# Kernel tuning notes

Measured on AMD Instinct MI355X. Metric: run time of the kernel, lower is better.

The kernel has to match this reference:

```python
import jax, jax.numpy as jnp
import numpy as np

B, N, C, H, P = 8, 4096, 256, 4, 64  # batch, tokens, hidden, heads, proj_size


def setup_inputs() -> dict:
    key = jax.random.key(0)
    ks = jax.random.split(key, 6)
    sc = 0.02
    x = jax.random.normal(ks[0], (B, N, C), jnp.float32)
    bank = jax.random.normal(ks[1], (B, N, C), jnp.float32)  # unused by forward, kept for fidelity
    W_qkvv = jax.random.normal(ks[2], (4 * C, C), jnp.float32) * sc  # Linear(C, 4C), no bias
    W_E = jax.random.normal(ks[3], (P, N), jnp.float32) * sc          # E = F shared Linear(N, P)
    b_E = jnp.zeros((P,), jnp.float32)
    temperature = jnp.ones((H, 1, 1), jnp.float32)
    temperature2 = jnp.ones((H, 1, 1), jnp.float32)
    W_out1 = jax.random.normal(ks[4], (C // 2, C), jnp.float32) * sc  # out_proj (spatial branch)
    b_out1 = jnp.zeros((C // 2,), jnp.float32)
    W_out2 = jax.random.normal(ks[5], (C // 2, C), jnp.float32) * sc  # out_proj2 (channel branch)
    b_out2 = jnp.zeros((C // 2,), jnp.float32)
    prelu_a = jnp.array(0.25, jnp.float32)  # nn.PReLU() default: single shared slope
    return {"x": x, "bank": bank, "W_qkvv": W_qkvv, "W_E": W_E, "b_E": b_E,
            "temperature": temperature, "temperature2": temperature2,
            "W_out1": W_out1, "b_out1": b_out1, "W_out2": W_out2, "b_out2": b_out2,
            "prelu_a": prelu_a}


def _l2norm(t):
    # torch F.normalize(dim=-1): x / max(||x||_2, eps)
    return t / jnp.maximum(jnp.linalg.norm(t, axis=-1, keepdims=True), 1e-12)


def reference(x, bank, W_qkvv, W_E, b_E, temperature, temperature2,
              W_out1, b_out1, W_out2, b_out2, prelu_a):
    Bb, Nn, Cc = x.shape
    Hh = temperature.shape[0]
    d = Cc // Hh
    # qkvv projection -> [4, B, H, N, d], then transpose token/feature axes -> [B, H, d, N]
    qkvv = (x @ W_qkvv.T).reshape(Bb, Nn, 4, Hh, d).transpose(2, 0, 3, 1, 4)
    q, k, v_ca, v_sa = (qkvv[0].transpose(0, 1, 3, 2), qkvv[1].transpose(0, 1, 3, 2),
                        qkvv[2].transpose(0, 1, 3, 2), qkvv[3].transpose(0, 1, 3, 2))
    # shared linear E=F projects the token axis N -> P (applied to UNnormalized k, v_sa)
    k_proj = jnp.einsum('bhdn,pn->bhdp', k, W_E) + b_E      # [B,H,d,P]
    v_sa_proj = jnp.einsum('bhdn,pn->bhdp', v_sa, W_E) + b_E  # [B,H,d,P]
    qn = _l2norm(q)
    kn = _l2norm(k)
    # channel attention: [B,H,d,d]
    attn_ca = jax.nn.softmax(jnp.einsum('bhdn,bhen->bhde', qn, kn) * temperature, axis=-1)
    x_ca = jnp.einsum('bhde,bhen->bhdn', attn_ca, v_ca).transpose(0, 3, 1, 2).reshape(Bb, Nn, Cc)
    # spatial attention (projected): [B,H,N,P]
    attn_sa = jax.nn.softmax(jnp.einsum('bhdn,bhdp->bhnp', qn, k_proj) * temperature2, axis=-1)
    x_sa = jnp.einsum('bhnp,bhdp->bhnd', attn_sa, v_sa_proj).transpose(0, 2, 1, 3).reshape(Bb, Nn, Cc)
    x_sa = x_sa @ W_out1.T + b_out1
    x_ca = x_ca @ W_out2.T + b_out2
    out = jnp.concatenate([x_sa, x_ca], axis=-1)
    return jnp.where(out >= 0, out, prelu_a * out)  # PReLU
```

## Files before the change

### kernel.cpp

```cpp
#include <hip/hip_runtime.h>
#include <cstdint>
#include <cstddef>

constexpr int B_ = 8, N_ = 4096, C_ = 256, H_ = 4, D_ = 64, P_ = 64;
constexpr int OC_ = 4 * C_;
constexpr int M_  = B_ * N_;
constexpr int GX_ROWS = 320;
constexpr int KS_G = 8;
constexpr int XT_TILES = M_ / 64;

#define DEV_INLINE __device__ __forceinline__

typedef unsigned short ushort_t;
typedef __attribute__((ext_vector_type(8))) short short8;
typedef __attribute__((ext_vector_type(4))) short short4v;
typedef __attribute__((ext_vector_type(4))) float floatx4;

DEV_INLINE short f2bf(float f) {
  unsigned int u = __builtin_bit_cast(unsigned int, f);
  u += 0x7FFFu + ((u >> 16) & 1u);
  return (short)(u >> 16);
}
DEV_INLINE float bf2f(ushort_t u) {
  return __builtin_bit_cast(float, (unsigned int)u << 16);
}
DEV_INLINE short4v cvt4(float4 v) {
  short4v s = {f2bf(v.x), f2bf(v.y), f2bf(v.z), f2bf(v.w)};
  return s;
}

__global__ __launch_bounds__(256) void k_cast(const float* __restrict__ x,
                                              const float* __restrict__ Wq,
                                              const float* __restrict__ WE,
                                              const float* __restrict__ W1,
                                              const float* __restrict__ W2,
                                              ushort_t* __restrict__ xt,
                                              ushort_t* __restrict__ wqb,
                                              ushort_t* __restrict__ web,
                                              ushort_t* __restrict__ w1b,
                                              ushort_t* __restrict__ w2b) {
  const int t = threadIdx.x;
  if (blockIdx.x >= XT_TILES) {
    constexpr size_t WQ4 = (size_t)OC_ * C_ / 4;
    constexpr size_t WE4 = (size_t)P_ * N_ / 4;
    constexpr size_t W14 = (size_t)128 * C_ / 4;
    constexpr size_t TOTW4 = WQ4 + WE4 + 2 * W14;
    const size_t stride = (size_t)128 * 256;
    for (size_t i = (size_t)(blockIdx.x - XT_TILES) * 256 + t; i < TOTW4; i += stride) {
      const float* src; ushort_t* dst; size_t o;
      if (i < WQ4) { src = Wq; dst = wqb; o = i; }
      else if (i < WQ4 + WE4) { src = WE; dst = web; o = i - WQ4; }
      else if (i < WQ4 + WE4 + W14) { src = W1; dst = w1b; o = i - WQ4 - WE4; }
      else { src = W2; dst = w2b; o = i - WQ4 - WE4 - W14; }
      float4 v = ((const float4*)src)[o];
      *(short4v*)&dst[o * 4] = cvt4(v);
    }
    return;
  }
  __shared__ __align__(16) short Xs[64 * 264];
  const int n0 = blockIdx.x * 64;
  const int b = n0 >> 12, nl = n0 & 4095;
#pragma unroll
  for (int rep = 0; rep < 16; ++rep) {
    const int f4 = rep * 256 + t;
    const int row = f4 >> 6, c4 = f4 & 63;
    float4 v = *(const float4*)&x[(size_t)(n0 + row) * 256 + c4 * 4];
    *(short4v*)&Xs[row * 264 + c4 * 4] = cvt4(v);
  }
  __syncthreads();
  const int ch = t;
  ushort_t* dst = &xt[((size_t)b * 256 + ch) * 4096 + nl];
#pragma unroll
  for (int g = 0; g < 8; ++g) {
    short8 o;
#pragma unroll
    for (int i = 0; i < 8; ++i) o[i] = Xs[(g * 8 + i) * 264 + ch];
    *(short8*)&dst[g * 8] = o;
  }
}

__global__ __launch_bounds__(512) void k_gram(const ushort_t* __restrict__ xt,
                                              const ushort_t* __restrict__ web,
                                              float* __restrict__ Gxp) {
  __shared__ __align__(16) short As[128 * 72];
  __shared__ __align__(16) short Bs[256 * 72];
  const int job = blockIdx.x;
  const int y = blockIdx.y;
  const int b = y >> 3, ksp = y & 7;
  const int t = threadIdx.x;
  const int oc = t & 7, rr = t >> 3;
  const int lane = t & 63, wave = t >> 6;
  const int m16 = lane & 15, quad = lane >> 4;
  const int wm = (wave >> 2) << 6, wn = (wave & 3) << 6;
  const ushort_t* Asrc = (job < 2)
      ? xt + (size_t)(b * 256 + job * 128) * 4096 : web;
  const ushort_t* Bsrc = xt + (size_t)b * 256 * 4096;
  floatx4 acc[4][4];
#pragma unroll
  for (int i = 0; i < 4; ++i)
#pragma unroll
    for (int j = 0; j < 4; ++j) acc[i][j] = (floatx4)(0.f);
#pragma unroll 1
  for (int it = 0; it < 8; ++it) {
    const int n0 = ksp * 512 + it * 64;
    short8 a8[2], b8[4];
#pragma unroll
    for (int rp = 0; rp < 2; ++rp) {
      int ar = rr + 64 * rp;
      if (job == 2) ar &= 63;
      a8[rp] = *(const short8*)&Asrc[(size_t)ar * 4096 + n0 + 8 * oc];
    }
#pragma unroll
    for (int rp = 0; rp < 4; ++rp)
      b8[rp] = *(const short8*)&Bsrc[(size_t)(rr + 64 * rp) * 4096 + n0 + 8 * oc];
    __syncthreads();
#pragma unroll
    for (int rp = 0; rp < 2; ++rp)
      *(short8*)&As[(rr + 64 * rp) * 72 + 8 * oc] = a8[rp];
#pragma unroll
    for (int rp = 0; rp < 4; ++rp)
      *(short8*)&Bs[(rr + 64 * rp) * 72 + 8 * oc] = b8[rp];
    __syncthreads();
#pragma unroll
    for (int ks = 0; ks < 2; ++ks) {
      if (job < 2) {
        short8 af[4], bf[4];
#pragma unroll
        for (int i = 0; i < 4; ++i)
          af[i] = *(const short8*)&As[(wm + i * 16 + m16) * 72 + ks * 32 + quad * 8];
#pragma unroll
        for (int j = 0; j < 4; ++j)
          bf[j] = *(const short8*)&Bs[(wn + j * 16 + m16) * 72 + ks * 32 + quad * 8];
#pragma unroll
        for (int i = 0; i < 4; ++i)
#pragma unroll
          for (int j = 0; j < 4; ++j)
            acc[i][j] = __builtin_amdgcn_mfma_f32_16x16x32_bf16(af[i], bf[j], acc[i][j], 0, 0, 0);
      } else {
        short8 af[4], bf[2];
#pragma unroll
        for (int i = 0; i < 4; ++i)
          af[i] = *(const short8*)&As[(i * 16 + m16) * 72 + ks * 32 + quad * 8];
#pragma unroll
        for (int j = 0; j < 2; ++j)
          bf[j] = *(const short8*)&Bs[(wave * 32 + j * 16 + m16) * 72 + ks * 32 + quad * 8];
#pragma unroll
        for (int i = 0; i < 4; ++i)
#pragma unroll
          for (int j = 0; j < 2; ++j)
            acc[i][j] = __builtin_amdgcn_mfma_f32_16x16x32_bf16(af[i], bf[j], acc[i][j], 0, 0, 0);
      }
    }
  }
  float* pb = Gxp + (size_t)y * (GX_ROWS * 256);
  if (job < 2) {
#pragma unroll
    for (int i = 0; i < 4; ++i)
#pragma unroll
      for (int r = 0; r < 4; ++r) {
        const int grow = job * 128 + wm + i * 16 + quad * 4 + r;
#pragma unroll
        for (int j = 0; j < 4; ++j)
          pb[(size_t)grow * 256 + wn + j * 16 + m16] = acc[i][j][r];
      }
  } else {
#pragma unroll
    for (int i = 0; i < 4; ++i)
#pragma unroll
      for (int r = 0; r < 4; ++r) {
        const int grow = 256 + i * 16 + quad * 4 + r;
#pragma unroll
        for (int j = 0; j < 2; ++j)
          pb[(size_t)grow * 256 + wave * 32 + j * 16 + m16] = acc[i][j][r];
      }
  }
}

__global__ __launch_bounds__(256) void k_gred(const float* __restrict__ Gxp,
                                              float* __restrict__ Gx) {
  const int i = blockIdx.x * 256 + threadIdx.x;
  constexpr int PB4 = GX_ROWS * 256 / 4;
  const int fb = i / PB4, rem = i - fb * PB4;
  const float4* p = (const float4*)Gxp;
  float4 s = p[(size_t)fb * KS_G * PB4 + rem];
#pragma unroll
  for (int k = 1; k < KS_G; ++k) {
    float4 v = p[((size_t)fb * KS_G + k) * PB4 + rem];
    s.x += v.x; s.y += v.y; s.z += v.z; s.w += v.w;
  }
  ((float4*)Gx)[i] = s;
}

__global__ __launch_bounds__(256) void k_mid1(const ushort_t* __restrict__ wqb,
                                              const float* __restrict__ Gx,
                                              ushort_t* __restrict__ T2b,
                                              float* __restrict__ ssq) {
  __shared__ __align__(16) short As[128 * 72];
  __shared__ __align__(16) short Bs[128 * 72];
  const int bm = blockIdx.x * 128;
  const int b  = blockIdx.y >> 1;
  const int jb = blockIdx.y & 1;
  const int t = threadIdx.x;
  const int oc = t & 7;
  const int rr = t >> 3;
  const int lane = t & 63, wave = t >> 6;
  const int m16 = lane & 15, quad = lane >> 4;
  const int wm = (wave >> 1) << 6, wn = (wave & 1) << 6;
  const float* Bsrc = Gx + ((size_t)b * GX_ROWS + jb * 128) * 256;
  floatx4 acc[4][4];
#pragma unroll
  for (int i = 0; i < 4; ++i)
#pragma unroll
    for (int j = 0; j < 4; ++j) acc[i][j] = (floatx4)(0.f);
#pragma unroll 1
  for (int k0 = 0; k0 < 256; k0 += 64) {
    short8 a8[4], b8[4];
#pragma unroll
    for (int j = 0; j < 4; ++j) {
      const int r = rr + 32 * j;
      a8[j] = *(const short8*)&wqb[(size_t)(bm + r) * 256 + k0 + 8 * oc];
      float4 g0 = *(const float4*)&Bsrc[(size_t)r * 256 + k0 + 8 * oc];
      float4 g1 = *(const float4*)&Bsrc[(size_t)r * 256 + k0 + 8 * oc + 4];
      short8 bb;
      bb[0] = f2bf(g0.x); bb[1] = f2bf(g0.y); bb[2] = f2bf(g0.z); bb[3] = f2bf(g0.w);
      bb[4] = f2bf(g1.x); bb[5] = f2bf(g1.y); bb[6] = f2bf(g1.z); bb[7] = f2bf(g1.w);
      b8[j] = bb;
    }
    __syncthreads();
#pragma unroll
    for (int j = 0; j < 4; ++j) {
      const int r = rr + 32 * j;
      *(short8*)&As[r * 72 + 8 * oc] = a8[j];
      *(short8*)&Bs[r * 72 + 8 * oc] = b8[j];
    }
    __syncthreads();
#pragma unroll
    for (int ks = 0; ks < 2; ++ks) {
      short8 af[4], bf[4];
#pragma unroll
      for (int i = 0; i < 4; ++i)
        af[i] = *(const short8*)&As[(wm + i * 16 + m16) * 72 + ks * 32 + quad * 8];
#pragma unroll
      for (int j = 0; j < 4; ++j)
        bf[j] = *(const short8*)&Bs[(wn + j * 16 + m16) * 72 + ks * 32 + quad * 8];
#pragma unroll
      for (int i = 0; i < 4; ++i)
#pragma unroll
        for (int j = 0; j < 4; ++j)
          acc[i][j] = __builtin_amdgcn_mfma_f32_16x16x32_bf16(af[i], bf[j], acc[i][j], 0, 0, 0);
    }
  }
#pragma unroll
  for (int i = 0; i < 4; ++i)
#pragma unroll
    for (int r = 0; r < 4; ++r) {
      const int gr = bm + wm + i * 16 + quad * 4 + r;
      float s = 0.f;
#pragma unroll
      for (int j = 0; j < 4; ++j) {
        const int col = jb * 128 + wn + j * 16 + m16;
        T2b[((size_t)b * 512 + gr) * 256 + col] = (ushort_t)f2bf(acc[i][j][r]);
        s += bf2f(wqb[(size_t)gr * 256 + col]) * acc[i][j][r];
      }
      s += __shfl_xor(s, 1);
      s += __shfl_xor(s, 2);
      s += __shfl_xor(s, 4);
      s += __shfl_xor(s, 8);
      if (m16 == 0) atomicAdd(&ssq[b * 512 + gr], s);
    }
}

__global__ __launch_bounds__(256) void k_mid2(const ushort_t* __restrict__ wqb,
                                              const ushort_t* __restrict__ T2b,
                                              const float* __restrict__ Gx,
                                              const float* __restrict__ ssq,
                                              const float* __restrict__ bE,
                                              const float* __restrict__ t1,
                                              const float* __restrict__ t2,
                                              ushort_t* __restrict__ ab,
                                              ushort_t* __restrict__ ksb,
                                              ushort_t* __restrict__ vsb) {
  const int bh = blockIdx.x;
  const int job = blockIdx.y;
  const int b = bh >> 2, h = bh & 3;
  const int wave = threadIdx.x >> 6;
  const int lane = threadIdx.x & 63;
  const int m16 = lane & 15, quad = lane >> 4;
  const int Abase = (job == 0 ? 0 : (job == 1 ? 256 : 768)) + h * 64;
  const int arow = Abase + 16 * wave + m16;
  floatx4 acc[4];
#pragma unroll
  for (int j = 0; j < 4; ++j) acc[j] = (floatx4)(0.f);
#pragma unroll
  for (int ks = 0; ks < 8; ++ks) {
    const int boct = ks * 32 + quad * 8;
    short8 af = *(const short8*)&wqb[(size_t)arow * 256 + boct];
    short8 bf[4];
    if (job == 0) {
#pragma unroll
      for (int j = 0; j < 4; ++j)
        bf[j] = *(const short8*)&T2b[((size_t)b * 512 + 256 + h * 64 + 16 * j + m16) * 256 + boct];
    } else {
#pragma unroll
      for (int j = 0; j < 4; ++j) {
        const float* gp = Gx + ((size_t)b * GX_ROWS + 256 + 16 * j + m16) * 256 + boct;
        float4 g0 = *(const float4*)gp;
        float4 g1 = *(const float4*)(gp + 4);
        short8 bb;
        bb[0] = f2bf(g0.x); bb[1] = f2bf(g0.y); bb[2] = f2bf(g0.z); bb[3] = f2bf(g0.w);
        bb[4] = f2bf(g1.x); bb[5] = f2bf(g1.y); bb[6] = f2bf(g1.z); bb[7] = f2bf(g1.w);
        bf[j] = bb;
      }
    }
#pragma unroll
    for (int j = 0; j < 4; ++j)
      acc[j] = __builtin_amdgcn_mfma_f32_16x16x32_bf16(af, bf[j], acc[j], 0, 0, 0);
  }
  if (job == 0) {
    const float t1h = t1[h];
    float rnk[4];
#pragma unroll
    for (int j = 0; j < 4; ++j)
      rnk[j] = 1.f / fmaxf(sqrtf(ssq[b * 512 + 256 + h * 64 + 16 * j + m16]), 1e-12f);
#pragma unroll
    for (int r = 0; r < 4; ++r) {
      const int d = 16 * wave + quad * 4 + r;
      const float rq = 1.f / fmaxf(sqrtf(ssq[b * 512 + h * 64 + d]), 1e-12f);
      float l[4];
      float m = -1e30f;
#pragma unroll
      for (int j = 0; j < 4; ++j) {
        l[j] = acc[j][r] * rq * rnk[j] * t1h;
        m = fmaxf(m, l[j]);
      }
      m = fmaxf(m, __shfl_xor(m, 1));
      m = fmaxf(m, __shfl_xor(m, 2));
      m = fmaxf(m, __shfl_xor(m, 4));
      m = fmaxf(m, __shfl_xor(m, 8));
      float s = 0.f;
#pragma unroll
      for (int j = 0; j < 4; ++j) {
        l[j] = __expf(l[j] - m);
        s += l[j];
      }
      s += __shfl_xor(s, 1);
      s += __shfl_xor(s, 2);
      s += __shfl_xor(s, 4);
      s += __shfl_xor(s, 8);
      const float inv = 1.f / s;
#pragma unroll
      for (int j = 0; j < 4; ++j)
        ab[(size_t)bh * 4096 + d * 64 + 16 * j + m16] = (ushort_t)f2bf(l[j] * inv);
    }
  } else if (job == 1) {
    const float tt = t2[h];
#pragma unroll
    for (int r = 0; r < 4; ++r) {
      const int d = 16 * wave + quad * 4 + r;
      const float rq = 1.f / fmaxf(sqrtf(ssq[b * 512 + h * 64 + d]), 1e-12f);
#pragma unroll
      for (int j = 0; j < 4; ++j) {
        const int p = 16 * j + m16;
        ksb[(size_t)bh * 4096 + p * 64 + d] =
            (ushort_t)f2bf((acc[j][r] + bE[p]) * rq * tt);
      }
    }
  } else {
#pragma unroll
    for (int r = 0; r < 4; ++r) {
      const int d = 16 * wave + quad * 4 + r;
#pragma unroll
      for (int j = 0; j < 4; ++j) {
        const int p = 16 * j + m16;
        vsb[(size_t)bh * 4096 + d * 64 + p] = (ushort_t)f2bf(acc[j][r] + bE[p]);
      }
    }
  }
}

__global__ __launch_bounds__(256) void k_tok(const float* __restrict__ x,
                                             const ushort_t* __restrict__ wqb,
                                             const ushort_t* __restrict__ ab,
                                             const ushort_t* __restrict__ ksb,
                                             const ushort_t* __restrict__ vsb,
                                             const ushort_t* __restrict__ w1b,
                                             const float* __restrict__ b1,
                                             const ushort_t* __restrict__ w2b,
                                             const float* __restrict__ b2,
                                             const float* __restrict__ pa,
                                             float* __restrict__ out) {
  __shared__ __align__(16) short Xs[64 * 264];
  __shared__ __align__(16) short Qs[64 * 264];
  __shared__ __align__(16) short Vs[64 * 264];
  const int n0 = blockIdx.x * 64;
  const int b = n0 >> 12;
  const int t = threadIdx.x;
  const int lane = t & 63, wave = t >> 6;
  const int m16 = lane & 15, quad = lane >> 4;
  const int cw = wave * 64;
#pragma unroll
  for (int rep = 0; rep < 16; ++rep) {
    const int f4 = rep * 256 + t;
    const int row = f4 >> 6, c4 = f4 & 63;
    float4 v = *(const float4*)&x[(size_t)(n0 + row) * 256 + c4 * 4];
    *(short4v*)&Xs[row * 264 + c4 * 4] = cvt4(v);
  }
  __syncthreads();
#pragma unroll 1
  for (int pass = 0; pass < 2; ++pass) {
    const int wrow = (pass ? 512 : 0) + cw;
    short* dst = pass ? Vs : Qs;
    floatx4 acc[4][4];
#pragma unroll
    for (int i = 0; i < 4; ++i)
#pragma unroll
      for (int j = 0; j < 4; ++j) acc[i][j] = (floatx4)(0.f);
#pragma unroll
    for (int ks = 0; ks < 8; ++ks) {
      const int boct = ks * 32 + quad * 8;
      short8 af[4], bf[4];
#pragma unroll
      for (int i = 0; i < 4; ++i)
        af[i] = *(const short8*)&Xs[(16 * i + m16) * 264 + boct];
#pragma unroll
      for (int j = 0; j < 4; ++j)
        bf[j] = *(const short8*)&wqb[(size_t)(wrow + 16 * j + m16) * 256 + boct];
#pragma unroll
      for (int i = 0; i < 4; ++i)
#pragma unroll
        for (int j = 0; j < 4; ++j)
          acc[i][j] = __builtin_amdgcn_mfma_f32_16x16x32_bf16(af[i], bf[j], acc[i][j], 0, 0, 0);
    }
#pragma unroll
    for (int i = 0; i < 4; ++i)
#pragma unroll
      for (int r = 0; r < 4; ++r)
#pragma unroll
        for (int j = 0; j < 4; ++j)
          dst[(16 * i + quad * 4 + r) * 264 + cw + 16 * j + m16] =
              (short)f2bf(acc[i][j][r]);
  }
  __syncthreads();
  const int bh = b * 4 + wave;
  {
    floatx4 s[4][4];
#pragma unroll
    for (int i = 0; i < 4; ++i)
#pragma unroll
      for (int j = 0; j < 4; ++j) s[i][j] = (floatx4)(0.f);
#pragma unroll
    for (int ks = 0; ks < 2; ++ks) {
      const int boct = ks * 32 + quad * 8;
      short8 af[4], bf[4];
#pragma unroll
      for (int i = 0; i < 4; ++i)
        af[i] = *(const short8*)&Qs[(16 * i + m16) * 264 + cw + boct];
#pragma unroll
      for (int j = 0; j < 4; ++j)
        bf[j] = *(const short8*)&ksb[(size_t)bh * 4096 + (16 * j + m16) * 64 + boct];
#pragma unroll
      for (int i = 0; i < 4; ++i)
#pragma unroll
        for (int j = 0; j < 4; ++j)
          s[i][j] = __builtin_amdgcn_mfma_f32_16x16x32_bf16(af[i], bf[j], s[i][j], 0, 0, 0);
    }
#pragma unroll
    for (int i = 0; i < 4; ++i)
#pragma unroll
      for (int r = 0; r < 4; ++r) {
        float mr = fmaxf(fmaxf(s[i][0][r], s[i][1][r]), fmaxf(s[i][2][r], s[i][3][r]));
        mr = fmaxf(mr, __shfl_xor(mr, 1));
        mr = fmaxf(mr, __shfl_xor(mr, 2));
        mr = fmaxf(mr, __shfl_xor(mr, 4));
        mr = fmaxf(mr, __shfl_xor(mr, 8));
        float sr = 0.f;
#pragma unroll
        for (int j = 0; j < 4; ++j) {
          const float e = __expf(s[i][j][r] - mr);
          s[i][j][r] = e;
          sr += e;
        }
        sr += __shfl_xor(sr, 1);
        sr += __shfl_xor(sr, 2);
        sr += __shfl_xor(sr, 4);
        sr += __shfl_xor(sr, 8);
        const float inv = 1.f / sr;
#pragma unroll
        for (int j = 0; j < 4; ++j) s[i][j][r] *= inv;
      }
#pragma unroll
    for (int i = 0; i < 4; ++i)
#pragma unroll
      for (int r = 0; r < 4; ++r)
#pragma unroll
        for (int j = 0; j < 4; ++j)
          Qs[(16 * i + quad * 4 + r) * 264 + cw + 16 * j + m16] =
              (short)f2bf(s[i][j][r]);
    floatx4 o[4][4];
#pragma unroll
    for (int i = 0; i < 4; ++i)
#pragma unroll
      for (int j = 0; j < 4; ++j) o[i][j] = (floatx4)(0.f);
#pragma unroll
    for (int ks = 0; ks < 2; ++ks) {
      const int boct = ks * 32 + quad * 8;
      short8 af[4], bf[4];
#pragma unroll
      for (int i = 0; i < 4; ++i)
        af[i] = *(const short8*)&Qs[(16 * i + m16) * 264 + cw + boct];
#pragma unroll
      for (int j = 0; j < 4; ++j)
        bf[j] = *(const short8*)&vsb[(size_t)bh * 4096 + (16 * j + m16) * 64 + boct];
#pragma unroll
      for (int i = 0; i < 4; ++i)
#pragma unroll
        for (int j = 0; j < 4; ++j)
          o[i][j] = __builtin_amdgcn_mfma_f32_16x16x32_bf16(af[i], bf[j], o[i][j], 0, 0, 0);
    }
#pragma unroll
    for (int i = 0; i < 4; ++i)
#pragma unroll
      for (int r = 0; r < 4; ++r)
#pragma unroll
        for (int j = 0; j < 4; ++j)
          Xs[(16 * i + quad * 4 + r) * 264 + cw + 16 * j + m16] =
              (short)f2bf(o[i][j][r]);
  }
  {
    floatx4 o[4][4];
#pragma unroll
    for (int i = 0; i < 4; ++i)
#pragma unroll
      for (int j = 0; j < 4; ++j) o[i][j] = (floatx4)(0.f);
#pragma unroll
    for (int ks = 0; ks < 2; ++ks) {
      const int boct = ks * 32 + quad * 8;
      short8 af[4], bf[4];
#pragma unroll
      for (int i = 0; i < 4; ++i)
        af[i] = *(const short8*)&Vs[(16 * i + m16) * 264 + cw + boct];
#pragma unroll
      for (int j = 0; j < 4; ++j)
        bf[j] = *(const short8*)&ab[(size_t)bh * 4096 + (16 * j + m16) * 64 + boct];
#pragma unroll
      for (int i = 0; i < 4; ++i)
#pragma unroll
        for (int j = 0; j < 4; ++j)
          o[i][j] = __builtin_amdgcn_mfma_f32_16x16x32_bf16(af[i], bf[j], o[i][j], 0, 0, 0);
    }
#pragma unroll
    for (int i = 0; i < 4; ++i)
#pragma unroll
      for (int r = 0; r < 4; ++r)
#pragma unroll
        for (int j = 0; j < 4; ++j)
          Vs[(16 * i + quad * 4 + r) * 264 + cw + 16 * j + m16] =
              (short)f2bf(o[i][j][r]);
  }
  __syncthreads();
  {
    const short* Asrc = (wave < 2) ? Xs : Vs;
    const ushort_t* Wsrc = (wave < 2) ? w1b : w2b;
    const float* bias = (wave < 2) ? b1 : b2;
    const int wrow = (wave & 1) * 64;
    const int colbase = (wave < 2 ? 0 : 128) + wrow;
    floatx4 acc[4][4];
#pragma unroll
    for (int i = 0; i < 4; ++i)
#pragma unroll
      for (int j = 0; j < 4; ++j) acc[i][j] = (floatx4)(0.f);
#pragma unroll
    for (int ks = 0; ks < 8; ++ks) {
      const int boct = ks * 32 + quad * 8;
      short8 af[4], bf[4];
#pragma unroll
      for (int i = 0; i < 4; ++i)
        af[i] = *(const short8*)&Asrc[(16 * i + m16) * 264 + boct];
#pragma unroll
      for (int j = 0; j < 4; ++j)
        bf[j] = *(const short8*)&Wsrc[(size_t)(wrow + 16 * j + m16) * 256 + boct];
#pragma unroll
      for (int i = 0; i < 4; ++i)
#pragma unroll
        for (int j = 0; j < 4; ++j)
          acc[i][j] = __builtin_amdgcn_mfma_f32_16x16x32_bf16(af[i], bf[j], acc[i][j], 0, 0, 0);
    }
    const float slope = pa[0];
    float bj[4];
#pragma unroll
    for (int j = 0; j < 4; ++j) bj[j] = bias[wrow + 16 * j + m16];
#pragma unroll
    for (int i = 0; i < 4; ++i)
#pragma unroll
      for (int r = 0; r < 4; ++r) {
        const int gr = n0 + 16 * i + quad * 4 + r;
#pragma unroll
        for (int j = 0; j < 4; ++j) {
          float v = acc[i][j][r] + bj[j];
          v = v >= 0.f ? v : slope * v;
          out[(size_t)gr * C_ + colbase + 16 * j + m16] = v;
        }
      }
  }
}

extern "C" void kernel_launch(void* const* d_in, const int* in_sizes, int n_in,
                              void* d_out, int out_size, void* d_ws, size_t ws_size,
                              hipStream_t stream) {
  (void)in_sizes; (void)n_in; (void)out_size; (void)ws_size;
  const float* x  = (const float*)d_in[0];
  const float* Wq = (const float*)d_in[2];
  const float* WE = (const float*)d_in[3];
  const float* bE = (const float*)d_in[4];
  const float* t1 = (const float*)d_in[5];
  const float* t2 = (const float*)d_in[6];
  const float* W1 = (const float*)d_in[7];
  const float* b1 = (const float*)d_in[8];
  const float* W2 = (const float*)d_in[9];
  const float* b2 = (const float*)d_in[10];
  const float* pa = (const float*)d_in[11];
  float* out = (float*)d_out;

  float* ws = (float*)d_ws;
  size_t off = 0;
  float* Gx  = ws + off; off += (size_t)B_ * GX_ROWS * 256;
  float* ssq = ws + off; off += (size_t)B_ * 512;
  float* Gxp = ws + off; off += (size_t)KS_G * B_ * GX_ROWS * 256;
  ushort_t* ksb = (ushort_t*)(ws + off); off += 32 * 4096 / 2;
  ushort_t* vsb = (ushort_t*)(ws + off); off += 32 * 4096 / 2;
  ushort_t* ab  = (ushort_t*)(ws + off); off += 32 * 4096 / 2;
  ushort_t* xt  = (ushort_t*)(ws + off); off += (size_t)M_ * C_ / 2;
  ushort_t* wqb = (ushort_t*)(ws + off); off += (size_t)OC_ * C_ / 2;
  ushort_t* w1b = (ushort_t*)(ws + off); off += (size_t)128 * C_ / 2;
  ushort_t* w2b = (ushort_t*)(ws + off); off += (size_t)128 * C_ / 2;
  ushort_t* web = (ushort_t*)(ws + off); off += (size_t)P_ * N_ / 2;
  ushort_t* T2b = (ushort_t*)(ws + off); off += (size_t)B_ * 512 * C_ / 2;

  hipMemsetAsync(ssq, 0, (size_t)B_ * 512 * sizeof(float), stream);

  k_cast<<<XT_TILES + 128, 256, 0, stream>>>(x, Wq, WE, W1, W2,
                                             xt, wqb, web, w1b, w2b);
  k_gram<<<dim3(3, B_ * KS_G), 512, 0, stream>>>(xt, web, Gxp);
  k_gred<<<GX_ROWS * 256 * B_ / 4 / 256, 256, 0, stream>>>(Gxp, Gx);
  k_mid1<<<dim3(4, B_ * 2), 256, 0, stream>>>(wqb, Gx, T2b, ssq);
  k_mid2<<<dim3(32, 3), 256, 0, stream>>>(wqb, T2b, Gx, ssq, bE, t1, t2, ab, ksb, vsb);
  k_tok<<<M_ / 64, 256, 0, stream>>>(x, wqb, ab, ksb, vsb, w1b, b1, w2b, b2, pa, out);
}
```

Measured before the change: 227.5 us.

## Cut k_tok shared memory to two buffers and request two blocks per CU

Shared memory in the token kernel drops from three 64x264 bf16 buffers to two. The Q projection and spatial attention now run first, writing into Ys. The V_ca projection is then computed from Xs and overwrites Xs after a barrier. This lowers LDS per block and adds a launch-bounds minimum of two blocks, aiming for higher occupancy, but it reorders the stages and forces the compiler to fit registers under the tighter bound, which could cause spills.

```diff
diff --git a/kernel.cpp b/kernel.cpp
--- a/kernel.cpp
+++ b/kernel.cpp
@@ -378,26 +378,26 @@
   }
 }
 
-__global__ __launch_bounds__(256) void k_tok(const float* __restrict__ x,
-                                             const ushort_t* __restrict__ wqb,
-                                             const ushort_t* __restrict__ ab,
-                                             const ushort_t* __restrict__ ksb,
-                                             const ushort_t* __restrict__ vsb,
-                                             const ushort_t* __restrict__ w1b,
-                                             const float* __restrict__ b1,
-                                             const ushort_t* __restrict__ w2b,
-                                             const float* __restrict__ b2,
-                                             const float* __restrict__ pa,
-                                             float* __restrict__ out) {
+__global__ __launch_bounds__(256, 2) void k_tok(const float* __restrict__ x,
+                                                const ushort_t* __restrict__ wqb,
+                                                const ushort_t* __restrict__ ab,
+                                                const ushort_t* __restrict__ ksb,
+                                                const ushort_t* __restrict__ vsb,
+                                                const ushort_t* __restrict__ w1b,
+                                                const float* __restrict__ b1,
+                                                const ushort_t* __restrict__ w2b,
+                                                const float* __restrict__ b2,
+                                                const float* __restrict__ pa,
+                                                float* __restrict__ out) {
   __shared__ __align__(16) short Xs[64 * 264];
-  __shared__ __align__(16) short Qs[64 * 264];
-  __shared__ __align__(16) short Vs[64 * 264];
+  __shared__ __align__(16) short Ys[64 * 264];
   const int n0 = blockIdx.x * 64;
   const int b = n0 >> 12;
   const int t = threadIdx.x;
   const int lane = t & 63, wave = t >> 6;
   const int m16 = lane & 15, quad = lane >> 4;
   const int cw = wave * 64;
+  const int bh = b * 4 + wave;
 #pragma unroll
   for (int rep = 0; rep < 16; ++rep) {
     const int f4 = rep * 256 + t;
@@ -406,10 +406,7 @@
     *(short4v*)&Xs[row * 264 + c4 * 4] = cvt4(v);
   }
   __syncthreads();
-#pragma unroll 1
-  for (int pass = 0; pass < 2; ++pass) {
-    const int wrow = (pass ? 512 : 0) + cw;
-    short* dst = pass ? Vs : Qs;
+  {
     floatx4 acc[4][4];
 #pragma unroll
     for (int i = 0; i < 4; ++i)
@@ -424,7 +421,7 @@
         af[i] = *(const short8*)&Xs[(16 * i + m16) * 264 + boct];
 #pragma unroll
       for (int j = 0; j < 4; ++j)
-        bf[j] = *(const short8*)&wqb[(size_t)(wrow + 16 * j + m16) * 256 + boct];
+        bf[j] = *(const short8*)&wqb[(size_t)(cw + 16 * j + m16) * 256 + boct];
 #pragma unroll
       for (int i = 0; i < 4; ++i)
 #pragma unroll
@@ -437,11 +434,9 @@
       for (int r = 0; r < 4; ++r)
 #pragma unroll
         for (int j = 0; j < 4; ++j)
-          dst[(16 * i + quad * 4 + r) * 264 + cw + 16 * j + m16] =
+          Ys[(16 * i + quad * 4 + r) * 264 + cw + 16 * j + m16] =
               (short)f2bf(acc[i][j][r]);
   }
-  __syncthreads();
-  const int bh = b * 4 + wave;
   {
     floatx4 s[4][4];
 #pragma unroll
@@ -454,7 +449,7 @@
       short8 af[4], bf[4];
 #pragma unroll
       for (int i = 0; i < 4; ++i)
-        af[i] = *(const short8*)&Qs[(16 * i + m16) * 264 + cw + boct];
+        af[i] = *(const short8*)&Ys[(16 * i + m16) * 264 + cw + boct];
 #pragma unroll
       for (int j = 0; j < 4; ++j)
         bf[j] = *(const short8*)&ksb[(size_t)bh * 4096 + (16 * j + m16) * 64 + boct];
@@ -494,7 +489,7 @@
       for (int r = 0; r < 4; ++r)
 #pragma unroll
         for (int j = 0; j < 4; ++j)
-          Qs[(16 * i + quad * 4 + r) * 264 + cw + 16 * j + m16] =
+          Ys[(16 * i + quad * 4 + r) * 264 + cw + 16 * j + m16] =
               (short)f2bf(s[i][j][r]);
     floatx4 o[4][4];
 #pragma unroll
@@ -507,7 +502,7 @@
       short8 af[4], bf[4];
 #pragma unroll
       for (int i = 0; i < 4; ++i)
-        af[i] = *(const short8*)&Qs[(16 * i + m16) * 264 + cw + boct];
+        af[i] = *(const short8*)&Ys[(16 * i + m16) * 264 + cw + boct];
 #pragma unroll
       for (int j = 0; j < 4; ++j)
         bf[j] = *(const short8*)&vsb[(size_t)bh * 4096 + (16 * j + m16) * 64 + boct];
@@ -523,9 +518,39 @@
       for (int r = 0; r < 4; ++r)
 #pragma unroll
         for (int j = 0; j < 4; ++j)
-          Xs[(16 * i + quad * 4 + r) * 264 + cw + 16 * j + m16] =
+          Ys[(16 * i + quad * 4 + r) * 264 + cw + 16 * j + m16] =
               (short)f2bf(o[i][j][r]);
   }
+  floatx4 accv[4][4];
+#pragma unroll
+  for (int i = 0; i < 4; ++i)
+#pragma unroll
+    for (int j = 0; j < 4; ++j) accv[i][j] = (floatx4)(0.f);
+#pragma unroll
+  for (int ks = 0; ks < 8; ++ks) {
+    const int boct = ks * 32 + quad * 8;
+    short8 af[4], bf[4];
+#pragma unroll
+    for (int i = 0; i < 4; ++i)
+      af[i] = *(const short8*)&Xs[(16 * i + m16) * 264 + boct];
+#pragma unroll
+    for (int j = 0; j < 4; ++j)
+      bf[j] = *(const short8*)&wqb[(size_t)(512 + cw + 16 * j + m16) * 256 + boct];
+#pragma unroll
+    for (int i = 0; i < 4; ++i)
+#pragma unroll
+      for (int j = 0; j < 4; ++j)
+        accv[i][j] = __builtin_amdgcn_mfma_f32_16x16x32_bf16(af[i], bf[j], accv[i][j], 0, 0, 0);
+  }
+  __syncthreads();
+#pragma unroll
+  for (int i = 0; i < 4; ++i)
+#pragma unroll
+    for (int r = 0; r < 4; ++r)
+#pragma unroll
+      for (int j = 0; j < 4; ++j)
+        Xs[(16 * i + quad * 4 + r) * 264 + cw + 16 * j + m16] =
+            (short)f2bf(accv[i][j][r]);
   {
     floatx4 o[4][4];
 #pragma unroll
@@ -538,7 +563,7 @@
       short8 af[4], bf[4];
 #pragma unroll
       for (int i = 0; i < 4; ++i)
-        af[i] = *(const short8*)&Vs[(16 * i + m16) * 264 + cw + boct];
+        af[i] = *(const short8*)&Xs[(16 * i + m16) * 264 + cw + boct];
 #pragma unroll
       for (int j = 0; j < 4; ++j)
         bf[j] = *(const short8*)&ab[(size_t)bh * 4096 + (16 * j + m16) * 64 + boct];
@@ -554,12 +579,12 @@
       for (int r = 0; r < 4; ++r)
 #pragma unroll
         for (int j = 0; j < 4; ++j)
-          Vs[(16 * i + quad * 4 + r) * 264 + cw + 16 * j + m16] =
+          Xs[(16 * i + quad * 4 + r) * 264 + cw + 16 * j + m16] =
               (short)f2bf(o[i][j][r]);
   }
   __syncthreads();
   {
-    const short* Asrc = (wave < 2) ? Xs : Vs;
+    const short* Asrc = (wave < 2) ? Ys : Xs;
     const ushort_t* Wsrc = (wave < 2) ? w1b : w2b;
     const float* bias = (wave < 2) ? b1 : b2;
     const int wrow = (wave & 1) * 64;
```

Result: faster. 214.5 us (-5.7%).

## Fold Q and V_ca projections into per-batch weights, removing token-level qkvv GEMM

Applied to the files above, without the earlier changes.

Precomputes per-(batch,head) combined matrices: the scaled K projection is multiplied by W_q (Kc), and the channel-attention matrix by W_v and then by W_out2 (M2). The token kernel can then compute spatial scores directly from X and the channel branch directly from X with M2, skipping the 64x512x256 qkvv GEMM per tile. It also drops one LDS buffer and sets launch_bounds occupancy to 2. The cost is two small extra kernels, a larger K dimension in the score GEMM (256 instead of 64), and different bf16 rounding points.

```diff
diff --git a/kernel.cpp b/kernel.cpp
--- a/kernel.cpp
+++ b/kernel.cpp
@@ -38,8 +38,35 @@
                                               ushort_t* __restrict__ wqb,
                                               ushort_t* __restrict__ web,
                                               ushort_t* __restrict__ w1b,
-                                              ushort_t* __restrict__ w2b) {
+                                              ushort_t* __restrict__ w2b,
+                                              ushort_t* __restrict__ wqtq,
+                                              ushort_t* __restrict__ wv2t) {
+  __shared__ __align__(16) short Xs[64 * 264];
   const int t = threadIdx.x;
+  if (blockIdx.x >= XT_TILES + 128) {
+    const int tb = blockIdx.x - (XT_TILES + 128);
+    const int srcbase = (tb < 4 ? 0 : 512) + (tb & 3) * 64;
+    ushort_t* dstm = (tb < 4) ? wqtq : wv2t;
+    const int R = (tb & 3) * 64;
+#pragma unroll
+    for (int rep = 0; rep < 16; ++rep) {
+      const int f4 = rep * 256 + t;
+      const int row = f4 >> 6, c4 = f4 & 63;
+      float4 v = *(const float4*)&Wq[(size_t)(srcbase + row) * 256 + c4 * 4];
+      *(short4v*)&Xs[row * 264 + c4 * 4] = cvt4(v);
+    }
+    __syncthreads();
+    const int ch = t;
+    ushort_t* dst = &dstm[ch * 256 + R];
+#pragma unroll
+    for (int g = 0; g < 8; ++g) {
+      short8 o;
+#pragma unroll
+      for (int i = 0; i < 8; ++i) o[i] = Xs[(g * 8 + i) * 264 + ch];
+      *(short8*)&dst[g * 8] = o;
+    }
+    return;
+  }
   if (blockIdx.x >= XT_TILES) {
     constexpr size_t WQ4 = (size_t)OC_ * C_ / 4;
     constexpr size_t WE4 = (size_t)P_ * N_ / 4;
@@ -57,7 +84,6 @@
     }
     return;
   }
-  __shared__ __align__(16) short Xs[64 * 264];
   const int n0 = blockIdx.x * 64;
   const int b = n0 >> 12, nl = n0 & 4095;
 #pragma unroll
@@ -378,26 +404,118 @@
   }
 }
 
-__global__ __launch_bounds__(256) void k_tok(const float* __restrict__ x,
-                                             const ushort_t* __restrict__ wqb,
-                                             const ushort_t* __restrict__ ab,
-                                             const ushort_t* __restrict__ ksb,
-                                             const ushort_t* __restrict__ vsb,
-                                             const ushort_t* __restrict__ w1b,
-                                             const float* __restrict__ b1,
-                                             const ushort_t* __restrict__ w2b,
-                                             const float* __restrict__ b2,
-                                             const float* __restrict__ pa,
-                                             float* __restrict__ out) {
+__global__ __launch_bounds__(256) void k_mid3(const ushort_t* __restrict__ ksb,
+                                              const ushort_t* __restrict__ ab,
+                                              const ushort_t* __restrict__ wqtq,
+                                              const ushort_t* __restrict__ wv2t,
+                                              ushort_t* __restrict__ Kc,
+                                              ushort_t* __restrict__ AcT) {
+  const int bh = blockIdx.x;
+  const int job = blockIdx.y;
+  const int h = bh & 3;
+  const int wave = threadIdx.x >> 6;
+  const int lane = threadIdx.x & 63;
+  const int m16 = lane & 15, quad = lane >> 4;
+  const ushort_t* A = (job ? ab : ksb) + (size_t)bh * 4096;
+  const ushort_t* Bt = job ? wv2t : wqtq;
+  floatx4 acc[4][4];
+#pragma unroll
+  for (int i = 0; i < 4; ++i)
+#pragma unroll
+    for (int j = 0; j < 4; ++j) acc[i][j] = (floatx4)(0.f);
+#pragma unroll
+  for (int ks = 0; ks < 2; ++ks) {
+    const int boct = ks * 32 + quad * 8;
+    short8 af[4], bf[4];
+#pragma unroll
+    for (int i = 0; i < 4; ++i)
+      af[i] = *(const short8*)&A[(16 * i + m16) * 64 + boct];
+#pragma unroll
+    for (int j = 0; j < 4; ++j)
+      bf[j] = *(const short8*)&Bt[(size_t)(wave * 64 + 16 * j + m16) * 256 + h * 64 + boct];
+#pragma unroll
+    for (int i = 0; i < 4; ++i)
+#pragma unroll
+      for (int j = 0; j < 4; ++j)
+        acc[i][j] = __builtin_amdgcn_mfma_f32_16x16x32_bf16(af[i], bf[j], acc[i][j], 0, 0, 0);
+  }
+#pragma unroll
+  for (int i = 0; i < 4; ++i)
+#pragma unroll
+    for (int r = 0; r < 4; ++r) {
+      const int ar = 16 * i + quad * 4 + r;
+#pragma unroll
+      for (int j = 0; j < 4; ++j) {
+        const int cc = wave * 64 + 16 * j + m16;
+        if (job == 0)
+          Kc[(size_t)bh * 16384 + ar * 256 + cc] = (ushort_t)f2bf(acc[i][j][r]);
+        else
+          AcT[(size_t)bh * 16384 + cc * 64 + ar] = (ushort_t)f2bf(acc[i][j][r]);
+      }
+    }
+}
+
+__global__ __launch_bounds__(256) void k_mid4(const ushort_t* __restrict__ w2b,
+                                              const ushort_t* __restrict__ AcT,
+                                              ushort_t* __restrict__ M2) {
+  const int b = blockIdx.x;
+  const int ob = blockIdx.y * 64;
+  const int wave = threadIdx.x >> 6;
+  const int lane = threadIdx.x & 63;
+  const int m16 = lane & 15, quad = lane >> 4;
+  floatx4 acc[4][4];
+#pragma unroll
+  for (int i = 0; i < 4; ++i)
+#pragma unroll
+    for (int j = 0; j < 4; ++j) acc[i][j] = (floatx4)(0.f);
+#pragma unroll
+  for (int ks = 0; ks < 8; ++ks) {
+    const int boct = ks * 32 + quad * 8;
+    const int hsel = boct >> 6, de = boct & 63;
+    short8 af[4], bf[4];
+#pragma unroll
+    for (int i = 0; i < 4; ++i)
+      af[i] = *(const short8*)&w2b[(size_t)(ob + 16 * i + m16) * 256 + boct];
+#pragma unroll
+    for (int j = 0; j < 4; ++j)
+      bf[j] = *(const short8*)&AcT[((size_t)(b * 4 + hsel)) * 16384 +
+                                   (wave * 64 + 16 * j + m16) * 64 + de];
+#pragma unroll
+    for (int i = 0; i < 4; ++i)
+#pragma unroll
+      for (int j = 0; j < 4; ++j)
+        acc[i][j] = __builtin_amdgcn_mfma_f32_16x16x32_bf16(af[i], bf[j], acc[i][j], 0, 0, 0);
+  }
+#pragma unroll
+  for (int i = 0; i < 4; ++i)
+#pragma unroll
+    for (int r = 0; r < 4; ++r) {
+      const int oo = ob + 16 * i + quad * 4 + r;
+#pragma unroll
+      for (int j = 0; j < 4; ++j)
+        M2[(size_t)b * 32768 + oo * 256 + wave * 64 + 16 * j + m16] =
+            (ushort_t)f2bf(acc[i][j][r]);
+    }
+}
+
+__global__ __launch_bounds__(256, 2) void k_tok(const float* __restrict__ x,
+                                                const ushort_t* __restrict__ Kc,
+                                                const ushort_t* __restrict__ vsb,
+                                                const ushort_t* __restrict__ M2,
+                                                const ushort_t* __restrict__ w1b,
+                                                const float* __restrict__ b1,
+                                                const float* __restrict__ b2,
+                                                const float* __restrict__ pa,
+                                                float* __restrict__ out) {
   __shared__ __align__(16) short Xs[64 * 264];
-  __shared__ __align__(16) short Qs[64 * 264];
-  __shared__ __align__(16) short Vs[64 * 264];
+  __shared__ __align__(16) short Ys[64 * 264];
   const int n0 = blockIdx.x * 64;
   const int b = n0 >> 12;
   const int t = threadIdx.x;
   const int lane = t & 63, wave = t >> 6;
   const int m16 = lane & 15, quad = lane >> 4;
   const int cw = wave * 64;
+  const int bh = b * 4 + wave;
 #pragma unroll
   for (int rep = 0; rep < 16; ++rep) {
     const int f4 = rep * 256 + t;
@@ -406,15 +524,12 @@
     *(short4v*)&Xs[row * 264 + c4 * 4] = cvt4(v);
   }
   __syncthreads();
-#pragma unroll 1
-  for (int pass = 0; pass < 2; ++pass) {
-    const int wrow = (pass ? 512 : 0) + cw;
-    short* dst = pass ? Vs : Qs;
-    floatx4 acc[4][4];
-#pragma unroll
-    for (int i = 0; i < 4; ++i)
-#pragma unroll
-      for (int j = 0; j < 4; ++j) acc[i][j] = (floatx4)(0.f);
+  {
+    floatx4 s[4][4];
+#pragma unroll
+    for (int i = 0; i < 4; ++i)
+#pragma unroll
+      for (int j = 0; j < 4; ++j) s[i][j] = (floatx4)(0.f);
 #pragma unroll
     for (int ks = 0; ks < 8; ++ks) {
       const int boct = ks * 32 + quad * 8;
@@ -424,40 +539,7 @@
         af[i] = *(const short8*)&Xs[(16 * i + m16) * 264 + boct];
 #pragma unroll
       for (int j = 0; j < 4; ++j)
-        bf[j] = *(const short8*)&wqb[(size_t)(wrow + 16 * j + m16) * 256 + boct];
-#pragma unroll
-      for (int i = 0; i < 4; ++i)
-#pragma unroll
-        for (int j = 0; j < 4; ++j)
-          acc[i][j] = __builtin_amdgcn_mfma_f32_16x16x32_bf16(af[i], bf[j], acc[i][j], 0, 0, 0);
-    }
-#pragma unroll
-    for (int i = 0; i < 4; ++i)
-#pragma unroll
-      for (int r = 0; r < 4; ++r)
-#pragma unroll
-        for (int j = 0; j < 4; ++j)
-          dst[(16 * i + quad * 4 + r) * 264 + cw + 16 * j + m16] =
-              (short)f2bf(acc[i][j][r]);
-  }
-  __syncthreads();
-  const int bh = b * 4 + wave;
-  {
-    floatx4 s[4][4];
-#pragma unroll
-    for (int i = 0; i < 4; ++i)
-#pragma unroll
-      for (int j = 0; j < 4; ++j) s[i][j] = (floatx4)(0.f);
-#pragma unroll
-    for (int ks = 0; ks < 2; ++ks) {
-      const int boct = ks * 32 + quad * 8;
-      short8 af[4], bf[4];
-#pragma unroll
-      for (int i = 0; i < 4; ++i)
-        af[i] = *(const short8*)&Qs[(16 * i + m16) * 264 + cw + boct];
-#pragma unroll
-      for (int j = 0; j < 4; ++j)
-        bf[j] = *(const short8*)&ksb[(size_t)bh * 4096 + (16 * j + m16) * 64 + boct];
+        bf[j] = *(const short8*)&Kc[(size_t)bh * 16384 + (16 * j + m16) * 256 + boct];
 #pragma unroll
       for (int i = 0; i < 4; ++i)
 #pragma unroll
@@ -494,8 +576,10 @@
       for (int r = 0; r < 4; ++r)
 #pragma unroll
         for (int j = 0; j < 4; ++j)
-          Qs[(16 * i + quad * 4 + r) * 264 + cw + 16 * j + m16] =
+          Ys[(16 * i + quad * 4 + r) * 264 + cw + 16 * j + m16] =
               (short)f2bf(s[i][j][r]);
+  }
+  {
     floatx4 o[4][4];
 #pragma unroll
     for (int i = 0; i < 4; ++i)
@@ -507,7 +591,7 @@
       short8 af[4], bf[4];
 #pragma unroll
       for (int i = 0; i < 4; ++i)
-        af[i] = *(const short8*)&Qs[(16 * i + m16) * 264 + cw + boct];
+        af[i] = *(const short8*)&Ys[(16 * i + m16) * 264 + cw + boct];
 #pragma unroll
       for (int j = 0; j < 4; ++j)
         bf[j] = *(const short8*)&vsb[(size_t)bh * 4096 + (16 * j + m16) * 64 + boct];
@@ -523,44 +607,13 @@
       for (int r = 0; r < 4; ++r)
 #pragma unroll
         for (int j = 0; j < 4; ++j)
-          Xs[(16 * i + quad * 4 + r) * 264 + cw + 16 * j + m16] =
-              (short)f2bf(o[i][j][r]);
-  }
-  {
-    floatx4 o[4][4];
-#pragma unroll
-    for (int i = 0; i < 4; ++i)
-#pragma unroll
-      for (int j = 0; j < 4; ++j) o[i][j] = (floatx4)(0.f);
-#pragma unroll
-    for (int ks = 0; ks < 2; ++ks) {
-      const int boct = ks * 32 + quad * 8;
-      short8 af[4], bf[4];
-#pragma unroll
-      for (int i = 0; i < 4; ++i)
-        af[i] = *(const short8*)&Vs[(16 * i + m16) * 264 + cw + boct];
-#pragma unroll
-      for (int j = 0; j < 4; ++j)
-        bf[j] = *(const short8*)&ab[(size_t)bh * 4096 + (16 * j + m16) * 64 + boct];
-#pragma unroll
-      for (int i = 0; i < 4; ++i)
-#pragma unroll
-        for (int j = 0; j < 4; ++j)
-          o[i][j] = __builtin_amdgcn_mfma_f32_16x16x32_bf16(af[i], bf[j], o[i][j], 0, 0, 0);
-    }
-#pragma unroll
-    for (int i = 0; i < 4; ++i)
-#pragma unroll
-      for (int r = 0; r < 4; ++r)
-#pragma unroll
-        for (int j = 0; j < 4; ++j)
-          Vs[(16 * i + quad * 4 + r) * 264 + cw + 16 * j + m16] =
+          Ys[(16 * i + quad * 4 + r) * 264 + cw + 16 * j + m16] =
               (short)f2bf(o[i][j][r]);
   }
   __syncthreads();
   {
-    const short* Asrc = (wave < 2) ? Xs : Vs;
-    const ushort_t* Wsrc = (wave < 2) ? w1b : w2b;
+    const short* Asrc = (wave < 2) ? Ys : Xs;
+    const ushort_t* Wsrc = (wave < 2) ? w1b : (M2 + (size_t)b * 32768);
     const float* bias = (wave < 2) ? b1 : b2;
     const int wrow = (wave & 1) * 64;
     const int colbase = (wave < 2 ? 0 : 128) + wrow;
@@ -635,14 +688,21 @@
   ushort_t* w2b = (ushort_t*)(ws + off); off += (size_t)128 * C_ / 2;
   ushort_t* web = (ushort_t*)(ws + off); off += (size_t)P_ * N_ / 2;
   ushort_t* T2b = (ushort_t*)(ws + off); off += (size_t)B_ * 512 * C_ / 2;
+  ushort_t* wqtq = (ushort_t*)(ws + off); off += (size_t)256 * 256 / 2;
+  ushort_t* wv2t = (ushort_t*)(ws + off); off += (size_t)256 * 256 / 2;
+  ushort_t* Kc  = (ushort_t*)(ws + off); off += (size_t)32 * 16384 / 2;
+  ushort_t* AcT = (ushort_t*)(ws + off); off += (size_t)32 * 16384 / 2;
+  ushort_t* M2  = (ushort_t*)(ws + off); off += (size_t)B_ * 32768 / 2;
 
   hipMemsetAsync(ssq, 0, (size_t)B_ * 512 * sizeof(float), stream);
 
-  k_cast<<<XT_TILES + 128, 256, 0, stream>>>(x, Wq, WE, W1, W2,
-                                             xt, wqb, web, w1b, w2b);
+  k_cast<<<XT_TILES + 136, 256, 0, stream>>>(x, Wq, WE, W1, W2,
+                                             xt, wqb, web, w1b, w2b, wqtq, wv2t);
   k_gram<<<dim3(3, B_ * KS_G), 512, 0, stream>>>(xt, web, Gxp);
   k_gred<<<GX_ROWS * 256 * B_ / 4 / 256, 256, 0, stream>>>(Gxp, Gx);
   k_mid1<<<dim3(4, B_ * 2), 256, 0, stream>>>(wqb, Gx, T2b, ssq);
   k_mid2<<<dim3(32, 3), 256, 0, stream>>>(wqb, T2b, Gx, ssq, bE, t1, t2, ab, ksb, vsb);
-  k_tok<<<M_ / 64, 256, 0, stream>>>(x, wqb, ab, ksb, vsb, w1b, b1, w2b, b2, pa, out);
-}
+  k_mid3<<<dim3(32, 2), 256, 0, stream>>>(ksb, ab, wqtq, wv2t, Kc, AcT);
+  k_mid4<<<dim3(8, 2), 256, 0, stream>>>(w2b, AcT, M2);
+  k_tok<<<M_ / 64, 256, 0, stream>>>(x, Kc, vsb, M2, w1b, b1, b2, pa, out);
+}
```

Result: no change. 226.8 us (-0.3%).
